# Kernel tuning notes

Hardware: AMD Instinct MI355X
Metric: run time of the kernel (lower is better)

Reference implementation:

```python
import jax, jax.numpy as jnp
import numpy as np

N = 1_000_000
D_IN = 128
D_OUT = 128
S = 8192  # num_samples


def setup_inputs() -> dict:
    key = jax.random.key(0)
    k1, k2, k3, k4 = jax.random.split(key, 4)
    element_embeddings = jax.random.normal(k1, (N, D_IN), dtype=jnp.float32)
    w_att = jax.random.normal(k2, (D_IN,), dtype=jnp.float32) * (1.0 / np.sqrt(D_IN))
    w_out = jax.random.normal(k3, (D_OUT, D_IN), dtype=jnp.float32) * (1.0 / np.sqrt(D_IN))
    element_to_sample_map = jax.random.randint(k4, (N,), 0, S, dtype=jnp.int32)
    return {
        "element_embeddings": element_embeddings,
        "w_att": w_att,
        "w_out": w_out,
        "element_to_sample_map": element_to_sample_map,
        "num_samples": S,
    }


def reference(element_embeddings, w_att, w_out, element_to_sample_map, num_samples):
    idx = element_to_sample_map
    # attention scores: Linear(D_in, 1, bias=False) -> [N]
    scores = element_embeddings @ w_att  # [N]
    # scatter log-softmax over segments (eps=0), numerically stable
    seg_max = jax.ops.segment_max(scores, idx, num_segments=num_samples)  # [S]
    shifted = scores - seg_max[idx]  # [N]
    seg_sumexp = jax.ops.segment_sum(jnp.exp(shifted), idx, num_segments=num_samples)  # [S]
    attention_probs = jnp.exp(shifted - jnp.log(seg_sumexp)[idx])  # [N]
    # output projection then weighted scatter-sum pooling
    projected = element_embeddings @ w_out.T  # [N, D_out]
    return jax.ops.segment_sum(projected * attention_probs[:, None], idx, num_segments=num_samples)  # [S, D_out]
```

## Files before the change

kernel.cpp:

```cpp
#include <hip/hip_runtime.h>
#include <math.h>

#define CAP 256

__global__ __launch_bounds__(256) void k_scatterB(const int* __restrict__ idx,
                                                  int* __restrict__ cursor,
                                                  int* __restrict__ bucket, int n) {
    int i = blockIdx.x * 256 + threadIdx.x;
    if (i < n) {
        int s = idx[i];
        int pos = atomicAdd(&cursor[s], 1);
        if (pos < CAP) bucket[(size_t)s * CAP + pos] = i;
    }
}

__global__ __launch_bounds__(256, 4) void k_pool(
        const float* __restrict__ emb, const float* __restrict__ w_att,
        const int* __restrict__ cursor, const int* __restrict__ bucket,
        float* __restrict__ pooled, int S) {
    int wave = (blockIdx.x << 2) | (threadIdx.x >> 6);
    int lane = threadIdx.x & 63;
    if (wave >= S) return;
    int g   = lane >> 4;
    int l16 = lane & 15;
    int cnt = min(cursor[wave], CAP);
    const int* ob = bucket + (size_t)wave * CAP;
    const float* wrow = w_att + 8 * l16;
    float4 wa0 = *reinterpret_cast<const float4*>(wrow);
    float4 wa1 = *reinterpret_cast<const float4*>(wrow + 4);
    float4 a0 = make_float4(0.f, 0.f, 0.f, 0.f);
    float4 a1 = make_float4(0.f, 0.f, 0.f, 0.f);
    float Z = 0.f;
    if (cnt > 0) {
        int last = cnt - 1;
        int e = g;
        int i0 = ob[min(e, last)];
        const float* r = emb + (size_t)i0 * 128 + 8 * l16;
        float4 v0 = *reinterpret_cast<const float4*>(r);
        float4 v1 = *reinterpret_cast<const float4*>(r + 4);
        int nit = (cnt + 3) >> 2;
        for (int it = 0; it < nit; ++it) {
            int en = e + 4;
            int inext = ob[min(en, last)];
            const float* rn = emb + (size_t)inext * 128 + 8 * l16;
            float4 n0 = *reinterpret_cast<const float4*>(rn);
            float4 n1 = *reinterpret_cast<const float4*>(rn + 4);
            float part = v0.x * wa0.x + v0.y * wa0.y + v0.z * wa0.z + v0.w * wa0.w
                       + v1.x * wa1.x + v1.y * wa1.y + v1.z * wa1.z + v1.w * wa1.w;
            part += __shfl_xor(part, 1);
            part += __shfl_xor(part, 2);
            part += __shfl_xor(part, 4);
            part += __shfl_xor(part, 8);
            float ex = (e <= last) ? __expf(part) : 0.f;
            Z += ex;
            a0.x = fmaf(ex, v0.x, a0.x);
            a0.y = fmaf(ex, v0.y, a0.y);
            a0.z = fmaf(ex, v0.z, a0.z);
            a0.w = fmaf(ex, v0.w, a0.w);
            a1.x = fmaf(ex, v1.x, a1.x);
            a1.y = fmaf(ex, v1.y, a1.y);
            a1.z = fmaf(ex, v1.z, a1.z);
            a1.w = fmaf(ex, v1.w, a1.w);
            v0 = n0;
            v1 = n1;
            e = en;
        }
    }
#pragma unroll
    for (int m = 16; m <= 32; m <<= 1) {
        a0.x += __shfl_xor(a0.x, m);
        a0.y += __shfl_xor(a0.y, m);
        a0.z += __shfl_xor(a0.z, m);
        a0.w += __shfl_xor(a0.w, m);
        a1.x += __shfl_xor(a1.x, m);
        a1.y += __shfl_xor(a1.y, m);
        a1.z += __shfl_xor(a1.z, m);
        a1.w += __shfl_xor(a1.w, m);
        Z    += __shfl_xor(Z,    m);
    }
    float rn_ = (Z > 0.f) ? (1.0f / Z) : 0.f;
    if (g == 0) {
        float* o = pooled + (size_t)wave * 128 + 8 * l16;
        *reinterpret_cast<float4*>(o)     = make_float4(a0.x * rn_, a0.y * rn_, a0.z * rn_, a0.w * rn_);
        *reinterpret_cast<float4*>(o + 4) = make_float4(a1.x * rn_, a1.y * rn_, a1.z * rn_, a1.w * rn_);
    }
}

#define SPB 8
__global__ __launch_bounds__(256, 4) void k_proj(
        const float* __restrict__ w_out, float* __restrict__ io, int S) {
    __shared__ float wl[128][68];
    __shared__ float pl[SPB][64];
    int t = threadIdx.x;
    int d = t & 127;
    int h = t >> 7;
    int s0 = blockIdx.x * SPB;
    float acc[4] = {0.f, 0.f, 0.f, 0.f};

    for (int ph = 0; ph < 2; ++ph) {
        __syncthreads();
        for (int j = t; j < 2048; j += 256) {
            int r = j >> 4, c4 = j & 15;
            float4 wv = reinterpret_cast<const float4*>(w_out + (size_t)r * 128 + ph * 64)[c4];
            *reinterpret_cast<float4*>(&wl[r][c4 * 4]) = wv;
        }
        if (t < 128) {
            int sm = t >> 4, c4 = t & 15;
            int ss = s0 + sm;
            float4 pv = (ss < S)
                ? reinterpret_cast<const float4*>(io + (size_t)ss * 128 + ph * 64)[c4]
                : make_float4(0.f, 0.f, 0.f, 0.f);
            *reinterpret_cast<float4*>(&pl[sm][c4 * 4]) = pv;
        }
        __syncthreads();
#pragma unroll
        for (int k4 = 0; k4 < 16; ++k4) {
            float4 wv = *reinterpret_cast<const float4*>(&wl[d][k4 * 4]);
#pragma unroll
            for (int j = 0; j < 4; ++j) {
                float4 pv = *reinterpret_cast<const float4*>(&pl[2 * j + h][k4 * 4]);
                acc[j] = fmaf(wv.x, pv.x, acc[j]);
                acc[j] = fmaf(wv.y, pv.y, acc[j]);
                acc[j] = fmaf(wv.z, pv.z, acc[j]);
                acc[j] = fmaf(wv.w, pv.w, acc[j]);
            }
        }
    }
#pragma unroll
    for (int j = 0; j < 4; ++j) {
        int s = s0 + 2 * j + h;
        if (s < S) io[(size_t)s * 128 + d] = acc[j];
    }
}

extern "C" void kernel_launch(void* const* d_in, const int* in_sizes, int n_in,
                              void* d_out, int out_size, void* d_ws, size_t ws_size,
                              hipStream_t stream) {
    const float* emb   = (const float*)d_in[0];
    const float* w_att = (const float*)d_in[1];
    const float* w_out = (const float*)d_in[2];
    const int*   idx   = (const int*)d_in[3];
    const int N = in_sizes[0] / 128;
    const int S = out_size / 128;

    char* ws = (char*)d_ws;
    int* cursor = (int*)(ws + 0);
    int* bucket = (int*)(ws + 64 * 1024);
    float* out  = (float*)d_out;

    hipMemsetAsync(cursor, 0, (size_t)S * sizeof(int), stream);
    k_scatterB<<<(N + 255) / 256, 256, 0, stream>>>(idx, cursor, bucket, N);
    k_pool    <<<(S + 3) / 4, 256, 0, stream>>>(emb, w_att, cursor, bucket, out, S);
    k_proj    <<<(S + SPB - 1) / SPB, 256, 0, stream>>>(w_out, out, S);
}
```

Measured before the change: 299.3 us.

## Replace bucket-gather pooling with coalesced binning pass writing bf16 weighted rows

The per-sample bucket gather over random embedding rows is replaced with a counting sort into 512 coarse buckets. A streaming pass reads embeddings in order, computes exp scores, and writes exp-weighted rows as bf16 into bucket-sorted order. Partial softmax denominators are kept per block and then reduced. A per-bucket kernel accumulates the rows in shared memory with atomics, and the existing projection kernel runs afterwards. This aims to make the large embedding read coalesced, at the cost of an extra bf16 write and read of N×128, a loss of precision, and no max subtraction, so exp could overflow for large scores.

```diff
diff --git a/kernel.cpp b/kernel.cpp
--- a/kernel.cpp
+++ b/kernel.cpp
@@ -1,92 +1,153 @@
 #include <hip/hip_runtime.h>
 #include <math.h>
 
-#define CAP 256
-
-__global__ __launch_bounds__(256) void k_scatterB(const int* __restrict__ idx,
-                                                  int* __restrict__ cursor,
-                                                  int* __restrict__ bucket, int n) {
-    int i = blockIdx.x * 256 + threadIdx.x;
-    if (i < n) {
+#define NBB 256
+#define TBB 1024
+#define BK  512
+#define NS  8192
+#define SPB 8
+
+__device__ __forceinline__ unsigned int bf16rne(float f) {
+    unsigned int x = __float_as_uint(f);
+    return (x + 0x7FFFu + ((x >> 16) & 1u)) >> 16;
+}
+__device__ __forceinline__ float bf16tof(unsigned int u) {
+    return __uint_as_float(u << 16);
+}
+
+__global__ __launch_bounds__(TBB) void k_countC(const int* __restrict__ idx,
+                                                int* __restrict__ rb, int n) {
+    __shared__ int lh[BK];
+    int t = threadIdx.x, b = blockIdx.x;
+    if (t < BK) lh[t] = 0;
+    __syncthreads();
+    int chunk = (n + NBB - 1) / NBB;
+    int lo = b * chunk, hi = min(n, lo + chunk);
+    for (int i = lo + t; i < hi; i += TBB) atomicAdd(&lh[idx[i] >> 4], 1);
+    __syncthreads();
+    if (t < BK) rb[b * BK + t] = lh[t];
+}
+
+__global__ __launch_bounds__(BK) void k_scanB(int* __restrict__ rb,
+                                              int* __restrict__ bucketBase,
+                                              int* __restrict__ bucketCnt) {
+    __shared__ int sh[BK];
+    int t = threadIdx.x;
+    int run = 0;
+#pragma unroll 8
+    for (int b = 0; b < NBB; ++b) {
+        int v = rb[b * BK + t];
+        rb[b * BK + t] = run;
+        run += v;
+    }
+    bucketCnt[t] = run;
+    sh[t] = run;
+    __syncthreads();
+    for (int off = 1; off < BK; off <<= 1) {
+        int v = (t >= off) ? sh[t - off] : 0;
+        __syncthreads();
+        sh[t] += v;
+        __syncthreads();
+    }
+    bucketBase[t] = sh[t] - run;
+}
+
+__global__ __launch_bounds__(TBB) void k_bin(
+        const float* __restrict__ emb, const float* __restrict__ w_att,
+        const int* __restrict__ idx, const int* __restrict__ rb,
+        const int* __restrict__ bucketBase,
+        unsigned int* __restrict__ embh, unsigned char* __restrict__ sdx,
+        float* __restrict__ Zpart, int n) {
+    __shared__ int cur[BK];
+    __shared__ float Zf[NS];
+    int t = threadIdx.x, blk = blockIdx.x;
+    if (t < BK) cur[t] = bucketBase[t] + rb[blk * BK + t];
+    for (int s = t; s < NS; s += TBB) Zf[s] = 0.f;
+    __syncthreads();
+    int l16   = t & 15;
+    int lane  = t & 63;
+    int gbase = lane & ~15;
+    int gid   = t >> 4;
+    float4 wa0 = *reinterpret_cast<const float4*>(w_att + 4 * l16);
+    float4 wa1 = *reinterpret_cast<const float4*>(w_att + 64 + 4 * l16);
+    int chunk = (n + NBB - 1) / NBB;
+    int lo = blk * chunk, hi = min(n, lo + chunk);
+    for (int i = lo + gid; i < hi; i += 64) {
         int s = idx[i];
-        int pos = atomicAdd(&cursor[s], 1);
-        if (pos < CAP) bucket[(size_t)s * CAP + pos] = i;
-    }
-}
-
-__global__ __launch_bounds__(256, 4) void k_pool(
-        const float* __restrict__ emb, const float* __restrict__ w_att,
-        const int* __restrict__ cursor, const int* __restrict__ bucket,
-        float* __restrict__ pooled, int S) {
-    int wave = (blockIdx.x << 2) | (threadIdx.x >> 6);
-    int lane = threadIdx.x & 63;
-    if (wave >= S) return;
-    int g   = lane >> 4;
-    int l16 = lane & 15;
-    int cnt = min(cursor[wave], CAP);
-    const int* ob = bucket + (size_t)wave * CAP;
-    const float* wrow = w_att + 8 * l16;
-    float4 wa0 = *reinterpret_cast<const float4*>(wrow);
-    float4 wa1 = *reinterpret_cast<const float4*>(wrow + 4);
-    float4 a0 = make_float4(0.f, 0.f, 0.f, 0.f);
-    float4 a1 = make_float4(0.f, 0.f, 0.f, 0.f);
-    float Z = 0.f;
-    if (cnt > 0) {
-        int last = cnt - 1;
-        int e = g;
-        int i0 = ob[min(e, last)];
-        const float* r = emb + (size_t)i0 * 128 + 8 * l16;
-        float4 v0 = *reinterpret_cast<const float4*>(r);
-        float4 v1 = *reinterpret_cast<const float4*>(r + 4);
-        int nit = (cnt + 3) >> 2;
-        for (int it = 0; it < nit; ++it) {
-            int en = e + 4;
-            int inext = ob[min(en, last)];
-            const float* rn = emb + (size_t)inext * 128 + 8 * l16;
-            float4 n0 = *reinterpret_cast<const float4*>(rn);
-            float4 n1 = *reinterpret_cast<const float4*>(rn + 4);
-            float part = v0.x * wa0.x + v0.y * wa0.y + v0.z * wa0.z + v0.w * wa0.w
-                       + v1.x * wa1.x + v1.y * wa1.y + v1.z * wa1.z + v1.w * wa1.w;
-            part += __shfl_xor(part, 1);
-            part += __shfl_xor(part, 2);
-            part += __shfl_xor(part, 4);
-            part += __shfl_xor(part, 8);
-            float ex = (e <= last) ? __expf(part) : 0.f;
-            Z += ex;
-            a0.x = fmaf(ex, v0.x, a0.x);
-            a0.y = fmaf(ex, v0.y, a0.y);
-            a0.z = fmaf(ex, v0.z, a0.z);
-            a0.w = fmaf(ex, v0.w, a0.w);
-            a1.x = fmaf(ex, v1.x, a1.x);
-            a1.y = fmaf(ex, v1.y, a1.y);
-            a1.z = fmaf(ex, v1.z, a1.z);
-            a1.w = fmaf(ex, v1.w, a1.w);
-            v0 = n0;
-            v1 = n1;
-            e = en;
-        }
-    }
-#pragma unroll
-    for (int m = 16; m <= 32; m <<= 1) {
-        a0.x += __shfl_xor(a0.x, m);
-        a0.y += __shfl_xor(a0.y, m);
-        a0.z += __shfl_xor(a0.z, m);
-        a0.w += __shfl_xor(a0.w, m);
-        a1.x += __shfl_xor(a1.x, m);
-        a1.y += __shfl_xor(a1.y, m);
-        a1.z += __shfl_xor(a1.z, m);
-        a1.w += __shfl_xor(a1.w, m);
-        Z    += __shfl_xor(Z,    m);
-    }
-    float rn_ = (Z > 0.f) ? (1.0f / Z) : 0.f;
-    if (g == 0) {
-        float* o = pooled + (size_t)wave * 128 + 8 * l16;
-        *reinterpret_cast<float4*>(o)     = make_float4(a0.x * rn_, a0.y * rn_, a0.z * rn_, a0.w * rn_);
-        *reinterpret_cast<float4*>(o + 4) = make_float4(a1.x * rn_, a1.y * rn_, a1.z * rn_, a1.w * rn_);
-    }
-}
-
-#define SPB 8
+        const float* r = emb + (size_t)i * 128;
+        float4 v0 = *reinterpret_cast<const float4*>(r + 4 * l16);
+        float4 v1 = *reinterpret_cast<const float4*>(r + 64 + 4 * l16);
+        float part = v0.x * wa0.x + v0.y * wa0.y + v0.z * wa0.z + v0.w * wa0.w
+                   + v1.x * wa1.x + v1.y * wa1.y + v1.z * wa1.z + v1.w * wa1.w;
+        part += __shfl_xor(part, 1);
+        part += __shfl_xor(part, 2);
+        part += __shfl_xor(part, 4);
+        part += __shfl_xor(part, 8);
+        float ex = __expf(part);
+        int pos_ = 0;
+        if (l16 == 0) {
+            pos_ = atomicAdd(&cur[s >> 4], 1);
+            atomicAdd(&Zf[s], ex);
+        }
+        int pos = __shfl(pos_, gbase);
+        if (l16 == 0) sdx[pos] = (unsigned char)(s & 15);
+        uint4 o;
+        o.x = bf16rne(ex * v0.x) | (bf16rne(ex * v0.y) << 16);
+        o.y = bf16rne(ex * v0.z) | (bf16rne(ex * v0.w) << 16);
+        o.z = bf16rne(ex * v1.x) | (bf16rne(ex * v1.y) << 16);
+        o.w = bf16rne(ex * v1.z) | (bf16rne(ex * v1.w) << 16);
+        reinterpret_cast<uint4*>(embh)[(size_t)pos * 16 + l16] = o;
+    }
+    __syncthreads();
+    for (int s = t; s < NS; s += TBB) Zpart[(size_t)blk * NS + s] = Zf[s];
+}
+
+__global__ __launch_bounds__(256) void k_zred(const float* __restrict__ Zpart,
+                                              float* __restrict__ Z) {
+    int s = blockIdx.x * 256 + threadIdx.x;
+    float run = 0.f;
+#pragma unroll 8
+    for (int b = 0; b < NBB; ++b) run += Zpart[(size_t)b * NS + s];
+    Z[s] = run;
+}
+
+__global__ __launch_bounds__(256, 2) void k_acc(
+        const unsigned int* __restrict__ embh, const unsigned char* __restrict__ sdx,
+        const int* __restrict__ bucketBase, const int* __restrict__ bucketCnt,
+        const float* __restrict__ Z, float* __restrict__ out) {
+    __shared__ float acc[16 * 128];
+    int b = blockIdx.x, t = threadIdx.x;
+    for (int j = t; j < 2048; j += 256) acc[j] = 0.f;
+    __syncthreads();
+    int base = bucketBase[b], cnt = bucketCnt[b];
+    int l16 = t & 15, gid = t >> 4;
+    const uint4* eh = reinterpret_cast<const uint4*>(embh);
+    for (int r = gid; r < cnt; r += 16) {
+        int pos = base + r;
+        int sl  = sdx[pos];
+        uint4 o = eh[(size_t)pos * 16 + l16];
+        int sb  = sl * 128;
+        int rot = (8 * sl) & 127;
+        int d0  = 4 * l16, d1 = 64 + 4 * l16;
+        atomicAdd(&acc[sb + ((d0 + 0 + rot) & 127)], bf16tof(o.x & 0xFFFFu));
+        atomicAdd(&acc[sb + ((d0 + 1 + rot) & 127)], bf16tof(o.x >> 16));
+        atomicAdd(&acc[sb + ((d0 + 2 + rot) & 127)], bf16tof(o.y & 0xFFFFu));
+        atomicAdd(&acc[sb + ((d0 + 3 + rot) & 127)], bf16tof(o.y >> 16));
+        atomicAdd(&acc[sb + ((d1 + 0 + rot) & 127)], bf16tof(o.z & 0xFFFFu));
+        atomicAdd(&acc[sb + ((d1 + 1 + rot) & 127)], bf16tof(o.z >> 16));
+        atomicAdd(&acc[sb + ((d1 + 2 + rot) & 127)], bf16tof(o.w & 0xFFFFu));
+        atomicAdd(&acc[sb + ((d1 + 3 + rot) & 127)], bf16tof(o.w >> 16));
+    }
+    __syncthreads();
+    int s0 = b * 16;
+    for (int j = t; j < 2048; j += 256) {
+        int sl = j >> 7, d = j & 127;
+        float z = Z[s0 + sl];
+        float val = (z > 0.f) ? acc[sl * 128 + ((d + 8 * sl) & 127)] / z : 0.f;
+        out[(size_t)(s0 + sl) * 128 + d] = val;
+    }
+}
+
 __global__ __launch_bounds__(256, 4) void k_proj(
         const float* __restrict__ w_out, float* __restrict__ io, int S) {
     __shared__ float wl[128][68];
@@ -144,12 +205,20 @@
     const int S = out_size / 128;
 
     char* ws = (char*)d_ws;
-    int* cursor = (int*)(ws + 0);
-    int* bucket = (int*)(ws + 64 * 1024);
-    float* out  = (float*)d_out;
-
-    hipMemsetAsync(cursor, 0, (size_t)S * sizeof(int), stream);
-    k_scatterB<<<(N + 255) / 256, 256, 0, stream>>>(idx, cursor, bucket, N);
-    k_pool    <<<(S + 3) / 4, 256, 0, stream>>>(emb, w_att, cursor, bucket, out, S);
-    k_proj    <<<(S + SPB - 1) / SPB, 256, 0, stream>>>(w_out, out, S);
-}
+    int*   rb         = (int*)(ws + 0);
+    int*   bucketBase = (int*)(ws + 512 * 1024);
+    int*   bucketCnt  = (int*)(ws + 512 * 1024 + 8192);
+    float* Z          = (float*)(ws + 512 * 1024 + 16384);
+    float* Zpart      = (float*)(ws + 1024 * 1024);
+    unsigned char* sdx = (unsigned char*)(ws + 10 * 1024 * 1024);
+    unsigned int* embh = (unsigned int*)(ws + 16 * 1024 * 1024);
+    float* out = (float*)d_out;
+
+    k_countC<<<NBB, TBB, 0, stream>>>(idx, rb, N);
+    k_scanB <<<1, BK, 0, stream>>>(rb, bucketBase, bucketCnt);
+    k_bin   <<<NBB, TBB, 0, stream>>>(emb, w_att, idx, rb, bucketBase,
+                                      embh, sdx, Zpart, N);
+    k_zred  <<<NS / 256, 256, 0, stream>>>(Zpart, Z);
+    k_acc   <<<BK, 256, 0, stream>>>(embh, sdx, bucketBase, bucketCnt, Z, out);
+    k_proj  <<<(S + SPB - 1) / SPB, 256, 0, stream>>>(w_out, out, S);
+}
```

Result: slower. 981.6 us (+228.0%).
